# Performance work log

Hardware: AMD Instinct MI355X
Metric: run time of the kernel (lower is better)

Reference implementation:

```python
import jax, jax.numpy as jnp
import numpy as np

NUM_TAGS = 27
NEG = -100.0


def _build_tables():
    start = np.full(NUM_TAGS, NEG, np.float32)
    end = np.full(NUM_TAGS, NEG, np.float32)
    trans = np.full((NUM_TAGS, NUM_TAGS), NEG, np.float32)
    for i in [0, 5, 10, 15, 20, 25, 26]:
        start[i] = 0.0
    for i in range(4):
        for b in [0, 5, 10, 15, 20]:
            trans[b + i, b + 1 + i] = 0.0
    for i in [4, 9, 14, 19, 24]:
        trans[i, i] = 0.0
    trans[4, 26] = 0.0
    trans[9, 25] = 0.0
    trans[14, 26] = 0.0
    trans[19, 25] = 0.0
    trans[24, 25:] = 0.0
    trans[25, 0] = 0.0
    trans[25, 10] = 0.0
    trans[25, 25:] = 0.0
    trans[26, 5] = 0.0
    trans[26, 15] = 0.0
    trans[26, 25:] = 0.0
    for i in [4, 9, 14, 19, 24, 25, 26]:
        end[i] = 0.0
    repeats = np.array([10, 10, 5, 1, 1], np.int32)  # sums to 27
    mapping = np.repeat(np.arange(7), [5, 5, 5, 5, 5, 1, 1]).astype(np.int32)
    return jnp.asarray(start), jnp.asarray(end), jnp.asarray(trans), repeats, jnp.asarray(mapping)


def setup_inputs() -> dict:
    key = jax.random.key(0)
    B, C, L = 256, 5, 4096
    emissions = jax.random.normal(key, (B, C, L), dtype=jnp.float32)
    mask = jnp.ones((B, L), dtype=bool)
    return {"emissions": emissions, "mask": mask}


def reference(emissions, mask):
    start_t, end_t, trans, repeats, mapping = _build_tables()
    m = mask.T.astype(bool)                      # (L, B)
    em = jnp.transpose(emissions, (2, 0, 1))     # (L, B, 5)
    em = jnp.repeat(em, repeats, axis=2)         # (L, B, 27)
    L, B, T = em.shape

    score0 = start_t + em[0]                     # (B, T)

    def step(score, xs):
        em_i, m_i = xs
        # (B, prev, cur)
        ns = trans[None, :, :] + score[:, :, None] + em_i[:, None, :]
        idx = jnp.argmax(ns, axis=1).astype(jnp.int32)
        best = jnp.max(ns, axis=1)
        new_score = jnp.where(m_i[:, None], best, score)
        return new_score, idx

    score, hist = jax.lax.scan(step, score0, (em[1:], m[1:]))  # hist: (L-1, B, T)
    history = jnp.concatenate([hist, jnp.zeros((1, B, T), hist.dtype)], axis=0)  # (L, B, T)

    score = score + end_t
    end_tag = jnp.argmax(score, axis=1).astype(jnp.int32)       # (B,)
    seq_ends = m.sum(axis=0).astype(jnp.int32) - 1               # (B,)
    history = history.at[seq_ends, jnp.arange(B), :].set(end_tag[:, None])

    batch_idx = jnp.arange(B)

    def back(bt, h_row):
        bt = h_row[batch_idx, bt]
        return bt, bt

    _, tags = jax.lax.scan(back, jnp.zeros(B, jnp.int32), history, reverse=True)  # (L, B)
    decoded = tags.T                                             # (B, L)
    return mapping[decoded]
```

## Files before the change

### kernel.cpp

```cpp
#include <hip/hip_runtime.h>


constexpr int LQ = 4096;

__device__ const int PREV5[32][5] = {
  {25,25,25,25,25},{0,0,0,0,0},{1,1,1,1,1},{2,2,2,2,2},{3,4,3,3,3},
  {26,26,26,26,26},{5,5,5,5,5},{6,6,6,6,6},{7,7,7,7,7},{8,9,8,8,8},
  {25,25,25,25,25},{10,10,10,10,10},{11,11,11,11,11},{12,12,12,12,12},{13,14,13,13,13},
  {26,26,26,26,26},{15,15,15,15,15},{16,16,16,16,16},{17,17,17,17,17},{18,19,18,18,18},
  {20,20,20,20,20},{20,20,20,20,20},{21,21,21,21,21},{22,22,22,22,22},{23,24,23,23,23},
  {9,19,24,25,26},{4,14,24,25,26},
  {27,27,27,27,27},{28,28,28,28,28},{29,29,29,29,29},{30,30,30,30,30},{31,31,31,31,31}};
__device__ const float STARTV[32] = {
  0,-100,-100,-100,-100, 0,-100,-100,-100,-100, 0,-100,-100,-100,-100,
  0,-100,-100,-100,-100, 0,-100,-100,-100,-100, 0, 0, -100,-100,-100,-100,-100};
__device__ const float ENDVT[32] = {
  -100,-100,-100,-100,0, -100,-100,-100,-100,0, -100,-100,-100,-100,0,
  -100,-100,-100,-100,0, -100,-100,-100,-100,0, 0, 0, -100,-100,-100,-100,-100};
__device__ const int CHAN[32] = {
  0,0,0,0,0, 0,0,0,0,0, 1,1,1,1,1, 1,1,1,1,1, 2,2,2,2,2, 3, 4, 0,0,0,0,0};
__device__ const int SLOT[32] = {
  7,7,7,7,0, 7,7,7,7,1, 7,7,7,7,2, 7,7,7,7,3, 7,7,7,7,4, 5, 6, 7,7,7,7,7};

__device__ __forceinline__ float bperm(int addr, float v) {
  return __int_as_float(__builtin_amdgcn_ds_bpermute(addr, __float_as_int(v)));
}

__global__ __launch_bounds__(64, 1) void viterbi_fwd(const float* __restrict__ em,
                                                     unsigned char* __restrict__ H,
                                                     int* __restrict__ endtag) {
  const int lane = threadIdx.x;
  const int st = lane & 31;
  const int b = blockIdx.x * 2 + (lane >> 5);

  const int a0 = (PREV5[st][0] + (lane & 32)) << 2;
  const int a1 = (PREV5[st][1] + (lane & 32)) << 2;
  const int a2 = (PREV5[st][2] + (lane & 32)) << 2;
  const int a3 = (PREV5[st][3] + (lane & 32)) << 2;
  const int a4 = (PREV5[st][4] + (lane & 32)) << 2;
  const bool floorlane = (st == 20) || (st > 26);
  const float startv = STARTV[st];
  const float endv = ENDVT[st];

  const float* ep = em + ((size_t)b * 5 + CHAN[st]) * LQ;
  unsigned char* hp = H + (size_t)b * LQ * 8 + SLOT[st];

  float4 cur0 = *(const float4*)(ep + 0);
  float4 cur1 = *(const float4*)(ep + 4);

  float s = startv + cur0.x;

#define VSTEP(TOFF, EV)                                                        \
  {                                                                            \
    float p0 = bperm(a0, s), p1 = bperm(a1, s), p2 = bperm(a2, s),             \
          p3 = bperm(a3, s), p4 = bperm(a4, s);                                \
    float c0 = p0 + (EV), c1 = p1 + (EV), c2 = p2 + (EV),                      \
          c3 = p3 + (EV), c4 = p4 + (EV);                                      \
    float m = fmaxf(fmaxf(fmaxf(c0, c1), c2), fmaxf(c3, c4));                  \
    int cd = 4;                                                                \
    cd = (c3 == m) ? 3 : cd; cd = (c2 == m) ? 2 : cd;                          \
    cd = (c1 == m) ? 1 : cd; cd = (c0 == m) ? 0 : cd;                          \
    s = floorlane ? -1e30f : m;                                                \
    hp[(TOFF) * 8] = (unsigned char)cd;                                        \
  }

  {
    float4 n0 = *(const float4*)(ep + 8);
    float4 n1 = *(const float4*)(ep + 12);
    asm volatile("" ::: "memory");
    VSTEP(1, cur0.y) VSTEP(2, cur0.z) VSTEP(3, cur0.w)
    VSTEP(4, cur1.x) VSTEP(5, cur1.y) VSTEP(6, cur1.z) VSTEP(7, cur1.w)
    cur0 = n0; cur1 = n1;
    hp += 64;
  }
  for (int t0 = 8; t0 < LQ; t0 += 8) {
    const int tn = (t0 + 8 < LQ) ? (t0 + 8) : t0;
    float4 n0 = *(const float4*)(ep + tn);
    float4 n1 = *(const float4*)(ep + tn + 4);
    asm volatile("" ::: "memory");
    VSTEP(0, cur0.x) VSTEP(1, cur0.y) VSTEP(2, cur0.z) VSTEP(3, cur0.w)
    VSTEP(4, cur1.x) VSTEP(5, cur1.y) VSTEP(6, cur1.z) VSTEP(7, cur1.w)
    cur0 = n0; cur1 = n1;
    hp += 64;
  }
#undef VSTEP

  __shared__ float fs[64];
  fs[lane] = s + endv;
  __syncthreads();
  if ((lane & 31) == 0) {
    const int base = lane;
    float bb = fs[base]; int bi = 0;
#pragma unroll
    for (int j = 1; j < 27; ++j) {
      float v = fs[base + j];
      if (v > bb) { bb = v; bi = j; }
    }
    endtag[b] = bi;
  }
}

constexpr int SEG = 128;
constexpr int NSEG = LQ / SEG;

__device__ __forceinline__ int prevf(unsigned w, int s) {
  if (s == 25) { int c = (w >> 5) & 7;  return (c < 2) ? (9 + 10 * c) : (22 + c); }
  if (s == 26) { int c = (w >> 8) & 7;  return (c < 2) ? (4 + 10 * c) : (22 + c); }
  if (s < 25 && (s % 5) == 4) { int bit = (w >> (s / 5)) & 1; return bit ? s : s - 1; }
  if (s == 0 || s == 10) return 25;
  if (s == 5 || s == 15) return 26;
  return s - 1;
}

__device__ __forceinline__ int mapst(int s) { return (s < 25) ? (s / 5) : (s - 20); }

__global__ __launch_bounds__(896) void viterbi_back(const unsigned char* __restrict__ H,
                                                    const int* __restrict__ endtag,
                                                    int* __restrict__ out) {
  const int b = blockIdx.x;
  __shared__ __align__(16) unsigned W[LQ];
  __shared__ __align__(16) int tags[LQ];
  __shared__ signed char exS[NSEG][27];
  __shared__ int entryS[NSEG];

  const unsigned char* Hb = H + (size_t)b * LQ * 8;
  const int tid = threadIdx.x;

  for (int t = tid; t < LQ; t += 896) {
    uint2 v = *(const uint2*)(Hb + (size_t)t * 8);
    unsigned c4 = v.x & 0xffu, c9 = (v.x >> 8) & 0xffu,
             c14 = (v.x >> 16) & 0xffu, c19 = (v.x >> 24) & 0xffu,
             c24 = v.y & 0xffu, c25 = (v.y >> 8) & 0xffu, c26 = (v.y >> 16) & 0xffu;
    unsigned w = (unsigned)(c4 == 1) | ((unsigned)(c9 == 1) << 1) |
                 ((unsigned)(c14 == 1) << 2) | ((unsigned)(c19 == 1) << 3) |
                 ((unsigned)(c24 == 1) << 4) | (c25 << 5) | (c26 << 8);
    W[t] = w;
  }
  __syncthreads();

  const int seg = tid / 27;
  const int e = tid - seg * 27;

  if (tid < NSEG * 27) {
    const int lo = seg * SEG;
    const int hi = (seg == NSEG - 1) ? (LQ - 1) : (lo + SEG);
    int s = e;
    for (int t = hi; t > lo; --t) s = prevf(W[t], s);
    exS[seg][e] = (signed char)s;
  }
  __syncthreads();

  if (tid == 0) {
    int s = endtag[b];
    for (int k = NSEG - 1; k >= 0; --k) { entryS[k] = s; s = exS[k][s]; }
  }
  __syncthreads();

  if (tid < NSEG * 27 && e == entryS[seg]) {
    const int lo = seg * SEG;
    const int hi = (seg == NSEG - 1) ? (LQ - 1) : (lo + SEG);
    int s = e;
    if (seg == NSEG - 1) tags[LQ - 1] = mapst(s);
    for (int t = hi; t > lo; --t) {
      s = prevf(W[t], s);
      tags[t - 1] = mapst(s);
    }
  }
  __syncthreads();

  int4* outb = (int4*)(out + (size_t)b * LQ);
  const int4* tg = (const int4*)tags;
  for (int i = tid; i < LQ / 4; i += 896) outb[i] = tg[i];
}

extern "C" void kernel_launch(void* const* d_in, const int* in_sizes, int n_in,
                              void* d_out, int out_size, void* d_ws, size_t ws_size,
                              hipStream_t stream) {
  const float* em = (const float*)d_in[0];
  unsigned char* H = (unsigned char*)d_ws;
  int* endtag = (int*)((char*)d_ws + (9u << 20));
  int* out = (int*)d_out;

  viterbi_fwd<<<dim3(128), dim3(64), 0, stream>>>(em, H, endtag);
  viterbi_back<<<dim3(256), dim3(896), 0, stream>>>(H, endtag, out);
}
```

Before: 524.9 us.

## Pack eight sequences per wave with per-chain registers and DPP exchange

```diff
diff --git a/kernel.cpp b/kernel.cpp
--- a/kernel.cpp
+++ b/kernel.cpp
@@ -3,97 +3,113 @@
 
 constexpr int LQ = 4096;
 
-__device__ const int PREV5[32][5] = {
-  {25,25,25,25,25},{0,0,0,0,0},{1,1,1,1,1},{2,2,2,2,2},{3,4,3,3,3},
-  {26,26,26,26,26},{5,5,5,5,5},{6,6,6,6,6},{7,7,7,7,7},{8,9,8,8,8},
-  {25,25,25,25,25},{10,10,10,10,10},{11,11,11,11,11},{12,12,12,12,12},{13,14,13,13,13},
-  {26,26,26,26,26},{15,15,15,15,15},{16,16,16,16,16},{17,17,17,17,17},{18,19,18,18,18},
-  {20,20,20,20,20},{20,20,20,20,20},{21,21,21,21,21},{22,22,22,22,22},{23,24,23,23,23},
-  {9,19,24,25,26},{4,14,24,25,26},
-  {27,27,27,27,27},{28,28,28,28,28},{29,29,29,29,29},{30,30,30,30,30},{31,31,31,31,31}};
-__device__ const float STARTV[32] = {
-  0,-100,-100,-100,-100, 0,-100,-100,-100,-100, 0,-100,-100,-100,-100,
-  0,-100,-100,-100,-100, 0,-100,-100,-100,-100, 0, 0, -100,-100,-100,-100,-100};
-__device__ const float ENDVT[32] = {
-  -100,-100,-100,-100,0, -100,-100,-100,-100,0, -100,-100,-100,-100,0,
-  -100,-100,-100,-100,0, -100,-100,-100,-100,0, 0, 0, -100,-100,-100,-100,-100};
-__device__ const int CHAN[32] = {
-  0,0,0,0,0, 0,0,0,0,0, 1,1,1,1,1, 1,1,1,1,1, 2,2,2,2,2, 3, 4, 0,0,0,0,0};
-__device__ const int SLOT[32] = {
-  7,7,7,7,0, 7,7,7,7,1, 7,7,7,7,2, 7,7,7,7,3, 7,7,7,7,4, 5, 6, 7,7,7,7,7};
-
-__device__ __forceinline__ float bperm(int addr, float v) {
-  return __int_as_float(__builtin_amdgcn_ds_bpermute(addr, __float_as_int(v)));
-}
+#define DPPF(vti, ctrl) \
+  __int_as_float(__builtin_amdgcn_update_dpp(0, (vti), (ctrl), 0xF, 0xF, true))
 
 __global__ __launch_bounds__(64, 1) void viterbi_fwd(const float* __restrict__ em,
                                                      unsigned char* __restrict__ H,
                                                      int* __restrict__ endtag) {
   const int lane = threadIdx.x;
-  const int st = lane & 31;
-  const int b = blockIdx.x * 2 + (lane >> 5);
-
-  const int a0 = (PREV5[st][0] + (lane & 32)) << 2;
-  const int a1 = (PREV5[st][1] + (lane & 32)) << 2;
-  const int a2 = (PREV5[st][2] + (lane & 32)) << 2;
-  const int a3 = (PREV5[st][3] + (lane & 32)) << 2;
-  const int a4 = (PREV5[st][4] + (lane & 32)) << 2;
-  const bool floorlane = (st == 20) || (st > 26);
-  const float startv = STARTV[st];
-  const float endv = ENDVT[st];
-
-  const float* ep = em + ((size_t)b * 5 + CHAN[st]) * LQ;
-  unsigned char* hp = H + (size_t)b * LQ * 8 + SLOT[st];
+  const int role = lane & 7;
+  const int b = blockIdx.x * 8 + (lane >> 3);
+  const bool ishub = (role == 5) || (role == 6);
+  const bool ishub26 = (role == 6);
+  const bool isR4 = (role == 4);
+  const bool headHi = (role < 2);
+
+  const int ch = (role < 2) ? 0 : (role < 4) ? 1 : (role == 4) ? 2
+               : (role == 5) ? 3 : (role == 6) ? 4 : 0;
+  const float* ep = em + ((size_t)b * 5 + ch) * LQ;
+  unsigned char* hp = H + (size_t)b * (LQ * 8) + role;
 
   float4 cur0 = *(const float4*)(ep + 0);
   float4 cur1 = *(const float4*)(ep + 4);
 
-  float s = startv + cur0.x;
+  float s0, s1, s2, s3, s4, vt;
+  {
+    const float e = cur0.x;
+    s0 = ((role < 5) ? 0.0f : (ishub ? 0.0f : -100.0f)) + e;
+    s1 = -100.0f + e; s2 = -100.0f + e; s3 = -100.0f + e;
+    s4 = ishub ? (0.0f + e) : (-100.0f + e);
+    vt = s4;
+  }
 
 #define VSTEP(TOFF, EV)                                                        \
   {                                                                            \
-    float p0 = bperm(a0, s), p1 = bperm(a1, s), p2 = bperm(a2, s),             \
-          p3 = bperm(a3, s), p4 = bperm(a4, s);                                \
-    float c0 = p0 + (EV), c1 = p1 + (EV), c2 = p2 + (EV),                      \
-          c3 = p3 + (EV), c4 = p4 + (EV);                                      \
-    float m = fmaxf(fmaxf(fmaxf(c0, c1), c2), fmaxf(c3, c4));                  \
+    const float e = (EV);                                                      \
+    const int vti = __float_as_int(vt);                                        \
+    const float g1 = DPPF(vti, 0x111);                             \
+    const float g2 = DPPF(vti, 0x112);                             \
+    const float g4 = DPPF(vti, 0x114);                             \
+    const float g6 = DPPF(vti, 0x116);                             \
+    const float h1 = DPPF(vti, 0x101);                             \
+    const float h3 = DPPF(vti, 0x103);                             \
+    const float h5 = DPPF(vti, 0x105);                             \
+               \
+    const float n1 = s0 + e, n2 = s1 + e, n3 = s2 + e;                         \
+    const float ta = s3 + e, tc = s4 + e;                                      \
+    const bool tg = tc > ta;                     \
+    const float ntail = tg ? tc : ta;                                          \
+    const float hsv = headHi ? h5 : h3;                  \
+    const float n0 = isR4 ? -1e30f : (hsv + e);        \
+           \
+    const float p0 = ishub26 ? g6 : g4;                   \
+    const float p1 = ishub26 ? g4 : g2;                   \
+    const float p2 = ishub26 ? g2 : g1;                   \
+    const float p3 = ishub26 ? g1 : vt;                   \
+    const float p4 = ishub26 ? vt : h1;                   \
+    const float c0 = p0 + e, c1 = p1 + e, c2 = p2 + e, c3 = p3 + e,            \
+                c4 = p4 + e;                                                   \
+    const float m = fmaxf(fmaxf(fmaxf(c0, c1), c2), fmaxf(c3, c4));            \
     int cd = 4;                                                                \
     cd = (c3 == m) ? 3 : cd; cd = (c2 == m) ? 2 : cd;                          \
     cd = (c1 == m) ? 1 : cd; cd = (c0 == m) ? 0 : cd;                          \
-    s = floorlane ? -1e30f : m;                                                \
-    hp[(TOFF) * 8] = (unsigned char)cd;                                        \
+    s0 = n0; s1 = n1; s2 = n2; s3 = n3;                                        \
+    const float nv = ishub ? m : ntail;                                        \
+    s4 = nv; vt = nv;                                                          \
+    hp[(TOFF) * 8] = (unsigned char)(ishub ? cd : (tg ? 1 : 0));               \
   }
 
   {
-    float4 n0 = *(const float4*)(ep + 8);
-    float4 n1 = *(const float4*)(ep + 12);
+    float4 n0v = *(const float4*)(ep + 8);
+    float4 n1v = *(const float4*)(ep + 12);
     asm volatile("" ::: "memory");
     VSTEP(1, cur0.y) VSTEP(2, cur0.z) VSTEP(3, cur0.w)
     VSTEP(4, cur1.x) VSTEP(5, cur1.y) VSTEP(6, cur1.z) VSTEP(7, cur1.w)
-    cur0 = n0; cur1 = n1;
+    cur0 = n0v; cur1 = n1v;
     hp += 64;
   }
   for (int t0 = 8; t0 < LQ; t0 += 8) {
     const int tn = (t0 + 8 < LQ) ? (t0 + 8) : t0;
-    float4 n0 = *(const float4*)(ep + tn);
-    float4 n1 = *(const float4*)(ep + tn + 4);
+    float4 n0v = *(const float4*)(ep + tn);
+    float4 n1v = *(const float4*)(ep + tn + 4);
     asm volatile("" ::: "memory");
     VSTEP(0, cur0.x) VSTEP(1, cur0.y) VSTEP(2, cur0.z) VSTEP(3, cur0.w)
     VSTEP(4, cur1.x) VSTEP(5, cur1.y) VSTEP(6, cur1.z) VSTEP(7, cur1.w)
-    cur0 = n0; cur1 = n1;
+    cur0 = n0v; cur1 = n1v;
     hp += 64;
   }
 #undef VSTEP
 
-  __shared__ float fs[64];
-  fs[lane] = s + endv;
-  __syncthreads();
-  if ((lane & 31) == 0) {
-    const int base = lane;
-    float bb = fs[base]; int bi = 0;
+  __shared__ float fs[8][27];
+  const int bl = lane >> 3;
+  if (role < 5) {
+    fs[bl][5 * role + 0] = s0 + (-100.0f);
+    fs[bl][5 * role + 1] = s1 + (-100.0f);
+    fs[bl][5 * role + 2] = s2 + (-100.0f);
+    fs[bl][5 * role + 3] = s3 + (-100.0f);
+    fs[bl][5 * role + 4] = s4 + 0.0f;
+  } else if (role == 5) {
+    fs[bl][25] = s4 + 0.0f;
+  } else if (role == 6) {
+    fs[bl][26] = s4 + 0.0f;
+  }
+  __syncthreads();
+  if (role == 0) {
+    float bb = fs[bl][0]; int bi = 0;
 #pragma unroll
     for (int j = 1; j < 27; ++j) {
-      float v = fs[base + j];
+      float v = fs[bl][j];
       if (v > bb) { bb = v; bi = j; }
     }
     endtag[b] = bi;
@@ -181,6 +197,6 @@
   int* endtag = (int*)((char*)d_ws + (9u << 20));
   int* out = (int*)d_out;
 
-  viterbi_fwd<<<dim3(128), dim3(64), 0, stream>>>(em, H, endtag);
+  viterbi_fwd<<<dim3(32), dim3(64), 0, stream>>>(em, H, endtag);
   viterbi_back<<<dim3(256), dim3(896), 0, stream>>>(H, endtag, out);
 }
```

New measurement: 656.3 us. +25.0%, slower.

## Software-pipeline argmax extraction and pack 3-bit backpointers into dwords

Applied to the files above, without the earlier changes.

```diff
diff --git a/kernel.cpp b/kernel.cpp
--- a/kernel.cpp
+++ b/kernel.cpp
@@ -8,15 +8,15 @@
   {26,26,26,26,26},{5,5,5,5,5},{6,6,6,6,6},{7,7,7,7,7},{8,9,8,8,8},
   {25,25,25,25,25},{10,10,10,10,10},{11,11,11,11,11},{12,12,12,12,12},{13,14,13,13,13},
   {26,26,26,26,26},{15,15,15,15,15},{16,16,16,16,16},{17,17,17,17,17},{18,19,18,18,18},
-  {20,20,20,20,20},{20,20,20,20,20},{21,21,21,21,21},{22,22,22,22,22},{23,24,23,23,23},
+  {31,31,31,31,31},{20,20,20,20,20},{21,21,21,21,21},{22,22,22,22,22},{23,24,23,23,23},
   {9,19,24,25,26},{4,14,24,25,26},
   {27,27,27,27,27},{28,28,28,28,28},{29,29,29,29,29},{30,30,30,30,30},{31,31,31,31,31}};
 __device__ const float STARTV[32] = {
   0,-100,-100,-100,-100, 0,-100,-100,-100,-100, 0,-100,-100,-100,-100,
-  0,-100,-100,-100,-100, 0,-100,-100,-100,-100, 0, 0, -100,-100,-100,-100,-100};
+  0,-100,-100,-100,-100, 0,-100,-100,-100,-100, 0, 0, 0,0,0,0,0};
 __device__ const float ENDVT[32] = {
   -100,-100,-100,-100,0, -100,-100,-100,-100,0, -100,-100,-100,-100,0,
-  -100,-100,-100,-100,0, -100,-100,-100,-100,0, 0, 0, -100,-100,-100,-100,-100};
+  -100,-100,-100,-100,0, -100,-100,-100,-100,0, 0, 0, 0,0,0,0,0};
 __device__ const int CHAN[32] = {
   0,0,0,0,0, 0,0,0,0,0, 1,1,1,1,1, 1,1,1,1,1, 2,2,2,2,2, 3, 4, 0,0,0,0,0};
 __device__ const int SLOT[32] = {
@@ -27,7 +27,7 @@
 }
 
 __global__ __launch_bounds__(64, 1) void viterbi_fwd(const float* __restrict__ em,
-                                                     unsigned char* __restrict__ H,
+                                                     unsigned* __restrict__ Hd,
                                                      int* __restrict__ endtag) {
   const int lane = threadIdx.x;
   const int st = lane & 31;
@@ -38,52 +38,75 @@
   const int a2 = (PREV5[st][2] + (lane & 32)) << 2;
   const int a3 = (PREV5[st][3] + (lane & 32)) << 2;
   const int a4 = (PREV5[st][4] + (lane & 32)) << 2;
-  const bool floorlane = (st == 20) || (st > 26);
-  const float startv = STARTV[st];
+  const int slot = SLOT[st];
   const float endv = ENDVT[st];
 
   const float* ep = em + ((size_t)b * 5 + CHAN[st]) * LQ;
-  unsigned char* hp = H + (size_t)b * LQ * 8 + SLOT[st];
+  unsigned* hp = Hd + ((size_t)b << 12) + slot;
 
   float4 cur0 = *(const float4*)(ep + 0);
   float4 cur1 = *(const float4*)(ep + 4);
 
-  float s = startv + cur0.x;
-
-#define VSTEP(TOFF, EV)                                                        \
-  {                                                                            \
-    float p0 = bperm(a0, s), p1 = bperm(a1, s), p2 = bperm(a2, s),             \
-          p3 = bperm(a3, s), p4 = bperm(a4, s);                                \
-    float c0 = p0 + (EV), c1 = p1 + (EV), c2 = p2 + (EV),                      \
-          c3 = p3 + (EV), c4 = p4 + (EV);                                      \
-    float m = fmaxf(fmaxf(fmaxf(c0, c1), c2), fmaxf(c3, c4));                  \
-    int cd = 4;                                                                \
-    cd = (c3 == m) ? 3 : cd; cd = (c2 == m) ? 2 : cd;                          \
-    cd = (c1 == m) ? 1 : cd; cd = (c0 == m) ? 0 : cd;                          \
-    s = floorlane ? -1e30f : m;                                                \
-    hp[(TOFF) * 8] = (unsigned char)cd;                                        \
-  }
+  float s = (st > 26) ? -1e30f : (STARTV[st] + cur0.x);
+  float q0 = 0.f, q1 = 0.f, q2 = 0.f, q3 = 0.f, qm = 0.f;
+  unsigned cw = 0u;
+
+#define GATH() \
+  p0 = bperm(a0, s); p1 = bperm(a1, s); p2 = bperm(a2, s); \
+  p3 = bperm(a3, s); p4 = bperm(a4, s);
+#define EXTR(W, SH) { int cd = 4;                                   \
+  cd = (q3 == qm) ? 3 : cd; cd = (q2 == qm) ? 2 : cd;               \
+  cd = (q1 == qm) ? 1 : cd; cd = (q0 == qm) ? 0 : cd;               \
+  (W) |= ((unsigned)cd) << (SH); }
+#define CONS(EV) { const float e = (EV);                            \
+  const float c0 = p0 + e, c1 = p1 + e, c2 = p2 + e,                \
+              c3 = p3 + e, c4 = p4 + e;                             \
+  qm = fmaxf(fmaxf(fmaxf(fmaxf(c0, c1), c2), c3), c4);              \
+  q0 = c0; q1 = c1; q2 = c2; q3 = c3; s = qm; }
 
   {
     float4 n0 = *(const float4*)(ep + 8);
     float4 n1 = *(const float4*)(ep + 12);
     asm volatile("" ::: "memory");
-    VSTEP(1, cur0.y) VSTEP(2, cur0.z) VSTEP(3, cur0.w)
-    VSTEP(4, cur1.x) VSTEP(5, cur1.y) VSTEP(6, cur1.z) VSTEP(7, cur1.w)
+    float p0, p1, p2, p3, p4;
+    unsigned cwn = 0u;
+    GATH();               CONS(cur0.y);
+    GATH(); EXTR(cwn, 3); CONS(cur0.z);
+    GATH(); EXTR(cwn, 6); CONS(cur0.w);
+    GATH(); EXTR(cwn, 9); CONS(cur1.x);
+    GATH(); EXTR(cwn,12); CONS(cur1.y);
+    GATH(); EXTR(cwn,15); CONS(cur1.z);
+    GATH(); EXTR(cwn,18); CONS(cur1.w);
+    cw = cwn;
     cur0 = n0; cur1 = n1;
-    hp += 64;
-  }
-  for (int t0 = 8; t0 < LQ; t0 += 8) {
-    const int tn = (t0 + 8 < LQ) ? (t0 + 8) : t0;
+  }
+
+  for (int c = 1; c < 512; ++c) {
+    const int tn = (c < 511) ? ((c + 1) << 3) : (c << 3);
     float4 n0 = *(const float4*)(ep + tn);
     float4 n1 = *(const float4*)(ep + tn + 4);
     asm volatile("" ::: "memory");
-    VSTEP(0, cur0.x) VSTEP(1, cur0.y) VSTEP(2, cur0.z) VSTEP(3, cur0.w)
-    VSTEP(4, cur1.x) VSTEP(5, cur1.y) VSTEP(6, cur1.z) VSTEP(7, cur1.w)
+    float p0, p1, p2, p3, p4;
+    GATH();
+    EXTR(cw, 21);
+    if (slot < 7) hp[(c - 1) << 3] = cw;
+    CONS(cur0.x);
+    unsigned cwn = 0u;
+    GATH(); EXTR(cwn, 0); CONS(cur0.y);
+    GATH(); EXTR(cwn, 3); CONS(cur0.z);
+    GATH(); EXTR(cwn, 6); CONS(cur0.w);
+    GATH(); EXTR(cwn, 9); CONS(cur1.x);
+    GATH(); EXTR(cwn,12); CONS(cur1.y);
+    GATH(); EXTR(cwn,15); CONS(cur1.z);
+    GATH(); EXTR(cwn,18); CONS(cur1.w);
+    cw = cwn;
     cur0 = n0; cur1 = n1;
-    hp += 64;
-  }
-#undef VSTEP
+  }
+  EXTR(cw, 21);
+  if (slot < 7) hp[511 << 3] = cw;
+#undef GATH
+#undef EXTR
+#undef CONS
 
   __shared__ float fs[64];
   fs[lane] = s + endv;
@@ -114,7 +137,7 @@
 
 __device__ __forceinline__ int mapst(int s) { return (s < 25) ? (s / 5) : (s - 20); }
 
-__global__ __launch_bounds__(896) void viterbi_back(const unsigned char* __restrict__ H,
+__global__ __launch_bounds__(896) void viterbi_back(const unsigned* __restrict__ Hd,
                                                     const int* __restrict__ endtag,
                                                     int* __restrict__ out) {
   const int b = blockIdx.x;
@@ -123,18 +146,23 @@
   __shared__ signed char exS[NSEG][27];
   __shared__ int entryS[NSEG];
 
-  const unsigned char* Hb = H + (size_t)b * LQ * 8;
+  const unsigned* Hb = Hd + ((size_t)b << 12);
   const int tid = threadIdx.x;
 
-  for (int t = tid; t < LQ; t += 896) {
-    uint2 v = *(const uint2*)(Hb + (size_t)t * 8);
-    unsigned c4 = v.x & 0xffu, c9 = (v.x >> 8) & 0xffu,
-             c14 = (v.x >> 16) & 0xffu, c19 = (v.x >> 24) & 0xffu,
-             c24 = v.y & 0xffu, c25 = (v.y >> 8) & 0xffu, c26 = (v.y >> 16) & 0xffu;
-    unsigned w = (unsigned)(c4 == 1) | ((unsigned)(c9 == 1) << 1) |
-                 ((unsigned)(c14 == 1) << 2) | ((unsigned)(c19 == 1) << 3) |
-                 ((unsigned)(c24 == 1) << 4) | (c25 << 5) | (c26 << 8);
-    W[t] = w;
+  for (int c = tid; c < 512; c += 896) {
+    const uint4 q0 = *(const uint4*)(Hb + (c << 3));
+    const uint4 q1 = *(const uint4*)(Hb + (c << 3) + 4);
+    const unsigned d0 = q0.x, d1 = q0.y, d2 = q0.z, d3 = q0.w,
+                   d4 = q1.x, d5 = q1.y, d6 = q1.z;
+#pragma unroll
+    for (int j = 0; j < 8; ++j) {
+      const int sh = 3 * j;
+      unsigned w = ((d0 >> sh) & 1u) | (((d1 >> sh) & 1u) << 1) |
+                   (((d2 >> sh) & 1u) << 2) | (((d3 >> sh) & 1u) << 3) |
+                   (((d4 >> sh) & 1u) << 4) | (((d5 >> sh) & 7u) << 5) |
+                   (((d6 >> sh) & 7u) << 8);
+      W[(c << 3) + j] = w;
+    }
   }
   __syncthreads();
 
@@ -177,10 +205,10 @@
                               void* d_out, int out_size, void* d_ws, size_t ws_size,
                               hipStream_t stream) {
   const float* em = (const float*)d_in[0];
-  unsigned char* H = (unsigned char*)d_ws;
-  int* endtag = (int*)((char*)d_ws + (9u << 20));
+  unsigned* Hd = (unsigned*)d_ws;
+  int* endtag = (int*)((char*)d_ws + (5u << 20));
   int* out = (int*)d_out;
 
-  viterbi_fwd<<<dim3(128), dim3(64), 0, stream>>>(em, H, endtag);
-  viterbi_back<<<dim3(256), dim3(896), 0, stream>>>(H, endtag, out);
-}
+  viterbi_fwd<<<dim3(128), dim3(64), 0, stream>>>(em, Hd, endtag);
+  viterbi_back<<<dim3(256), dim3(896), 0, stream>>>(Hd, endtag, out);
+}
```

After: 518.7 us. Within noise of the previous version (-1.2%).
